# Performance work log

Hardware: AMD Instinct MI355X
Metric: run time of the kernel (lower is better)

The kernel has to match this reference:

```python
import jax, jax.numpy as jnp
import numpy as np

N = 50000      # nodes
E = 800000     # edges
D_IN = 128     # raw feature dim
H = 96         # hidden_channels
K = 8          # experts
L = 4          # num_layers
C = 40         # classes


def setup_inputs() -> dict:
    key = jax.random.key(0)
    ks = jax.random.split(key, 10)
    stdv = 1.0 / np.sqrt(H)
    inp = {
        'x': jax.random.normal(ks[0], (N, D_IN), dtype=jnp.float32),
        'edge_index': jax.random.randint(ks[1], (2, E), 0, N, dtype=jnp.int64),
        # fcs[0]: Linear(d, hidden); fcs[1]: Linear(hidden, c)
        'fc0_w': jax.random.normal(ks[2], (D_IN, H), dtype=jnp.float32) * 0.05,
        'fc0_b': jnp.zeros((H,), dtype=jnp.float32),
        'fc1_w': jax.random.normal(ks[3], (H, C), dtype=jnp.float32) * 0.05,
        'fc1_b': jnp.zeros((C,), dtype=jnp.float32),
        # context_enc (method='node'): per-layer Linear(hidden, K)
        'ctx_w': jax.random.normal(ks[4], (L, H, K), dtype=jnp.float32) * 0.05,
        'ctx_b': jnp.zeros((L, K), dtype=jnp.float32),
        # GraphMultiConvolution weights: [L, K, hidden, hidden], uniform(-stdv, stdv)
        'conv_w': jax.random.uniform(ks[5], (L, K, H, H), dtype=jnp.float32,
                                     minval=-stdv, maxval=stdv),
    }
    return inp


def reference(x, edge_index, fc0_w, fc0_b, fc1_w, fc1_b, ctx_w, ctx_b, conv_w):
    # eval-mode forward (training=False): no dropout, softmax routing
    row = edge_index[0]
    col = edge_index[1]
    h = jax.nn.relu(x @ fc0_w + fc0_b)                     # [N, H]
    for i in range(L):
        # routing logits and soft expert weights z: [N, K]
        z = jax.nn.softmax(h @ ctx_w[i] + ctx_b[i], axis=-1)
        # spmm aggregation: hi[r] = sum over edges (r, c) of h[c]
        hi = jax.ops.segment_sum(h[col], row, num_segments=N)  # [N, H]
        # K-expert batched matmul: [N, K, H]
        outs = jnp.einsum('nd,kdo->nko', hi, conv_w[i])
        # gumbel/softmax-weighted combine + residual
        out = jnp.einsum('nk,nko->no', z, outs) + h
        h = jax.nn.relu(out)
    return h @ fc1_w + fc1_b                               # [N, C]
```

## Files before the change

kernel.cpp:

```cpp
#include <hip/hip_runtime.h>

#define N_NODES 50000
#define N_EDGES 800000
#define DIN     128
#define H       96
#define HS      128
#define K_EXP   8
#define L_LAYERS 4
#define C_OUT   40

#define GSZ 6250

typedef _Float16 f16;
typedef f16 f16x2 __attribute__((ext_vector_type(2)));
typedef f16 f16x4 __attribute__((ext_vector_type(4)));
typedef f16 f16x8 __attribute__((ext_vector_type(8)));
typedef float f32x4 __attribute__((ext_vector_type(4)));


__global__ __launch_bounds__(256) void count_p(const int* __restrict__ row,
                                               int* __restrict__ deg,
                                               int* __restrict__ p, int e) {
    int i = blockIdx.x * blockDim.x + threadIdx.x;
    if (i < e) p[i] = atomicAdd(&deg[row[i]], 1);
}

__global__ __launch_bounds__(1024) void scanA(const int* __restrict__ deg,
                                              int* __restrict__ rowptr,
                                              int* __restrict__ partial, int n) {
    __shared__ int wsum[16];
    int tid  = threadIdx.x;
    int lane = tid & 63, wid = tid >> 6;
    int idx = blockIdx.x * 1024 + tid;
    int v = (idx < n) ? deg[idx] : 0;
    int s = v;
    #pragma unroll
    for (int off = 1; off < 64; off <<= 1) {
        int t = __shfl_up(s, off, 64);
        if (lane >= off) s += t;
    }
    if (lane == 63) wsum[wid] = s;
    __syncthreads();
    if (wid == 0 && lane < 16) {
        int w = wsum[lane];
        #pragma unroll
        for (int off = 1; off < 16; off <<= 1) {
            int t = __shfl_up(w, off, 16);
            if (lane >= off) w += t;
        }
        wsum[lane] = w;
    }
    __syncthreads();
    int waveoff = (wid == 0) ? 0 : wsum[wid - 1];
    if (idx < n) rowptr[idx + 1] = waveoff + s;
    if (tid == 1023) partial[blockIdx.x] = waveoff + s;
}

__global__ __launch_bounds__(1024) void scanC(int* __restrict__ rowptr,
                                              const int* __restrict__ partial,
                                              int nb, int n) {
    __shared__ int boff_s;
    int tid = threadIdx.x;
    if (tid < 64) {
        int v = 0;
        for (int j = tid; j < (int)blockIdx.x; j += 64) v += partial[j];
        #pragma unroll
        for (int off = 32; off >= 1; off >>= 1) v += __shfl_xor(v, off, 64);
        if (tid == 0) boff_s = v;
    }
    __syncthreads();
    int boff = boff_s;
    int idx = blockIdx.x * 1024 + tid;
    if (idx == 0) rowptr[0] = 0;
    if (idx < n) rowptr[idx + 1] += boff;
}

__global__ __launch_bounds__(256) void scatter_store_xcd(const int* __restrict__ row,
                                                         const int* __restrict__ col,
                                                         const int* __restrict__ p,
                                                         const int* __restrict__ rowptr,
                                                         int* __restrict__ csr, int e) {
    int g = blockIdx.x & 7;
    int rlo = g * GSZ, rhi = rlo + GSZ;
    int stride = (gridDim.x >> 3) * 256;
    for (int i = (blockIdx.x >> 3) * 256 + threadIdx.x; i < e; i += stride) {
        int r = row[i];
        if (r >= rlo && r < rhi)
            csr[rowptr[r] + p[i]] = col[i];
    }
}


#define CONV_TOT (L_LAYERS * K_EXP * H * H)
#define FC0_TOT  (DIN * H)
#define FC1_TOT  (48 * H)

__global__ void convert_all(const float* __restrict__ conv_w,
                            const float* __restrict__ fc0_w,
                            const float* __restrict__ fc1_w,
                            f16* __restrict__ wfrag, f16* __restrict__ fc0t,
                            f16* __restrict__ fc1t) {
    int i = blockIdx.x * blockDim.x + threadIdx.x;
    if (i < CONV_TOT) {
        int o = i % H;
        int t = i / H;
        int d = t % H;
        int lk = t / H;
        int ct = o >> 4, lc = o & 15;
        int ks = d >> 5, quad = (d >> 3) & 3, j = d & 7;
        wfrag[(size_t)lk * 9216 + ct * 1536 + ks * 512 + (quad * 16 + lc) * 8 + j] =
            (f16)conv_w[i];
    } else if (i < CONV_TOT + FC0_TOT) {
        int j = i - CONV_TOT;
        int o = j % H, d = j / H;
        fc0t[o * DIN + d] = (f16)fc0_w[j];
    } else if (i < CONV_TOT + FC0_TOT + FC1_TOT) {
        int j = i - CONV_TOT - FC0_TOT;
        int o = j / H, d = j % H;
        fc1t[j] = (o < C_OUT) ? (f16)fc1_w[d * C_OUT + o] : (f16)0.f;
    }
}


#define SPMM_BLOCKS ((N_NODES + 15) / 16)
#define CTX_BLOCKS  ((N_NODES + 255) / 256)

__global__ __launch_bounds__(256) void layer_pre(const f16* __restrict__ h16,
                                                 const int* __restrict__ rowptr,
                                                 const int* __restrict__ csr,
                                                 f16* __restrict__ hi16,
                                                 const float* __restrict__ cw,
                                                 const float* __restrict__ cb,
                                                 float* __restrict__ zt, int n) {
    __shared__ float ws[H * K_EXP];
    __shared__ float bs[K_EXP];
    int tid = threadIdx.x;
    if ((int)blockIdx.x < SPMM_BLOCKS) {
        int r  = blockIdx.x * 16 + (tid >> 4);
        int li = tid & 15;
        if (r >= n) return;
        int j = rowptr[r], e = rowptr[r + 1];
        float acc[8] = {};
        const f16* hb = h16 + li * 8;
        while (j < e) {
            int m = e - j; if (m > 16) m = 16;
            int c = 0;
            if (li < m) c = csr[j + li];
            int t = 0;
            for (; t + 4 <= m; t += 4) {
                int c0 = __shfl(c, t, 16),     c1 = __shfl(c, t + 1, 16);
                int c2 = __shfl(c, t + 2, 16), c3 = __shfl(c, t + 3, 16);
                f16x8 v0 = *(const f16x8*)(hb + (size_t)c0 * HS);
                f16x8 v1 = *(const f16x8*)(hb + (size_t)c1 * HS);
                f16x8 v2 = *(const f16x8*)(hb + (size_t)c2 * HS);
                f16x8 v3 = *(const f16x8*)(hb + (size_t)c3 * HS);
                #pragma unroll
                for (int q = 0; q < 8; q++) acc[q] += (float)v0[q];
                #pragma unroll
                for (int q = 0; q < 8; q++) acc[q] += (float)v1[q];
                #pragma unroll
                for (int q = 0; q < 8; q++) acc[q] += (float)v2[q];
                #pragma unroll
                for (int q = 0; q < 8; q++) acc[q] += (float)v3[q];
            }
            for (; t < m; t++) {
                int cc = __shfl(c, t, 16);
                f16x8 v = *(const f16x8*)(hb + (size_t)cc * HS);
                #pragma unroll
                for (int q = 0; q < 8; q++) acc[q] += (float)v[q];
            }
            j += m;
        }
        if (li < 12) {
            f16x8 o;
            #pragma unroll
            for (int q = 0; q < 8; q++) o[q] = (f16)acc[q];
            *(f16x8*)(hi16 + (size_t)r * HS + li * 8) = o;
        }
    } else {
        for (int t = tid; t < H * K_EXP; t += 256) ws[t] = cw[t];
        if (tid < K_EXP) bs[tid] = cb[tid];
        __syncthreads();
        int node = ((int)blockIdx.x - SPMM_BLOCKS) * 256 + tid;
        if (node >= n) return;
        float acc[K_EXP];
        #pragma unroll
        for (int k = 0; k < K_EXP; k++) acc[k] = bs[k];
        const f16* hr = h16 + (size_t)node * HS;
        #pragma unroll 3
        for (int c8 = 0; c8 < 12; c8++) {
            f16x8 v = *(const f16x8*)(hr + c8 * 8);
            #pragma unroll
            for (int j = 0; j < 8; j++) {
                float hv = (float)v[j];
                int d = c8 * 8 + j;
                #pragma unroll
                for (int k = 0; k < K_EXP; k++) acc[k] += hv * ws[d * K_EXP + k];
            }
        }
        float mx = acc[0];
        #pragma unroll
        for (int k = 1; k < K_EXP; k++) mx = fmaxf(mx, acc[k]);
        float s = 0.f;
        #pragma unroll
        for (int k = 0; k < K_EXP; k++) { acc[k] = __expf(acc[k] - mx); s += acc[k]; }
        float inv = 1.f / s;
        #pragma unroll
        for (int k = 0; k < K_EXP; k++)
            zt[(size_t)k * N_NODES + node] = acc[k] * inv;
    }
}


#define FPAD 136

__global__ __launch_bounds__(256) void fc0_kernel(const float* __restrict__ x,
                                                  const f16* __restrict__ fc0t,
                                                  const float* __restrict__ b,
                                                  f16* __restrict__ h16, int n) {
    __shared__ f16 As[64 * FPAD];
    __shared__ f16 Ws[96 * FPAD];
    int tid = threadIdx.x;
    int l = tid & 63, w = tid >> 6;
    int quad = l >> 4, lc = l & 15;
    int row0 = blockIdx.x * 64;

    for (int t = tid; t < 2048; t += 256) {
        int m = t >> 5, c4 = (t & 31) * 4;
        int gr = row0 + m;
        float4 v = {0.f, 0.f, 0.f, 0.f};
        if (gr < n) v = *(const float4*)(x + (size_t)gr * DIN + c4);
        f16x4 h4 = {(f16)v.x, (f16)v.y, (f16)v.z, (f16)v.w};
        *(f16x4*)&As[m * FPAD + c4] = h4;
    }
    for (int t = tid; t < 1536; t += 256) {
        int o = t >> 4, c8 = (t & 15) * 8;
        *(f16x8*)&Ws[o * FPAD + c8] = *(const f16x8*)(fc0t + o * DIN + c8);
    }
    __syncthreads();

    f16x8 afr[4];
    #pragma unroll
    for (int ks = 0; ks < 4; ks++)
        afr[ks] = *(const f16x8*)&As[(16 * w + lc) * FPAD + ks * 32 + quad * 8];

    f32x4 acc[6] = {};
    #pragma unroll
    for (int ct = 0; ct < 6; ct++) {
        #pragma unroll
        for (int ks = 0; ks < 4; ks++) {
            f16x8 bfr = *(const f16x8*)&Ws[(ct * 16 + lc) * FPAD + ks * 32 + quad * 8];
            acc[ct] = __builtin_amdgcn_mfma_f32_16x16x32_f16(afr[ks], bfr, acc[ct], 0, 0, 0);
        }
    }

    int m0 = 16 * w + quad * 4;
    #pragma unroll
    for (int r = 0; r < 4; r++) {
        int gr = row0 + m0 + r;
        if (gr < n) {
            #pragma unroll
            for (int ct = 0; ct < 6; ct++) {
                int o = ct * 16 + lc;
                h16[(size_t)gr * HS + o] = (f16)fmaxf(acc[ct][r] + b[o], 0.f);
            }
        }
    }
}


#define EG_STAGE 2
#define EG_HALFS (EG_STAGE * 9216)

__global__ __launch_bounds__(256) void expert_gemm(const f16* __restrict__ hi16,
                                                   const f16* __restrict__ hin16,
                                                   const f16* __restrict__ wfrag,
                                                   const float* __restrict__ zt,
                                                   f16* __restrict__ hout16, int n) {
    __shared__ f16 Wl[EG_HALFS];
    int tid = threadIdx.x;
    int l = tid & 63, w = tid >> 6;
    int quad = l >> 4, lc = l & 15;
    int wrow0 = blockIdx.x * 64 + w * 16;

    f16x8 afr[3];
    #pragma unroll
    for (int ks = 0; ks < 3; ks++)
        afr[ks] = *(const f16x8*)(hi16 + (size_t)(wrow0 + lc) * HS + ks * 32 + quad * 8);

    f32x4 acc[6] = {};

    for (int kb = 0; kb < K_EXP; kb += EG_STAGE) {
        __syncthreads();
        const f16* src = wfrag + (size_t)kb * 9216;
        for (int t = tid; t < EG_HALFS / 8; t += 256)
            *(f16x8*)&Wl[t * 8] = *(const f16x8*)(src + t * 8);
        __syncthreads();

        #pragma unroll
        for (int k2 = 0; k2 < EG_STAGE; k2++) {
            int k = kb + k2;
            f32x4 zf = *(const f32x4*)(zt + (size_t)k * N_NODES + wrow0 + quad * 4);
            #pragma unroll
            for (int ct = 0; ct < 6; ct++) {
                f16x8 b0 = *(const f16x8*)&Wl[k2 * 9216 + ct * 1536 + 0 * 512 + l * 8];
                f16x8 b1 = *(const f16x8*)&Wl[k2 * 9216 + ct * 1536 + 1 * 512 + l * 8];
                f16x8 b2 = *(const f16x8*)&Wl[k2 * 9216 + ct * 1536 + 2 * 512 + l * 8];
                f32x4 tmp = {};
                tmp = __builtin_amdgcn_mfma_f32_16x16x32_f16(afr[0], b0, tmp, 0, 0, 0);
                tmp = __builtin_amdgcn_mfma_f32_16x16x32_f16(afr[1], b1, tmp, 0, 0, 0);
                tmp = __builtin_amdgcn_mfma_f32_16x16x32_f16(afr[2], b2, tmp, 0, 0, 0);
                acc[ct] += zf * tmp;
            }
        }
    }

    #pragma unroll
    for (int r = 0; r < 4; r++) {
        int gr = wrow0 + quad * 4 + r;
        if (gr < n) {
            #pragma unroll
            for (int ct = 0; ct < 6; ct++) {
                int o = ct * 16 + lc;
                float v = fmaxf(acc[ct][r] + (float)hin16[(size_t)gr * HS + o], 0.f);
                hout16[(size_t)gr * HS + o] = (f16)v;
            }
        }
    }
}


#define APAD 104

__global__ __launch_bounds__(256) void fc1_kernel(const f16* __restrict__ h16,
                                                  const f16* __restrict__ fc1t,
                                                  const float* __restrict__ b,
                                                  float* __restrict__ out, int n) {
    __shared__ f16 As[64 * APAD];
    __shared__ f16 Ws[48 * APAD];
    int tid = threadIdx.x;
    int l = tid & 63, w = tid >> 6;
    int quad = l >> 4, lc = l & 15;
    int row0 = blockIdx.x * 64;

    for (int t = tid; t < 768; t += 256) {
        int m = t / 12, c8 = (t % 12) * 8;
        int gr = row0 + m;
        f16x8 v = {};
        if (gr < n) v = *(const f16x8*)(h16 + (size_t)gr * HS + c8);
        *(f16x8*)&As[m * APAD + c8] = v;
    }
    for (int t = tid; t < 576; t += 256) {
        int o = t / 12, c8 = (t % 12) * 8;
        *(f16x8*)&Ws[o * APAD + c8] = *(const f16x8*)(fc1t + o * H + c8);
    }
    __syncthreads();

    f16x8 afr[3];
    #pragma unroll
    for (int ks = 0; ks < 3; ks++)
        afr[ks] = *(const f16x8*)&As[(16 * w + lc) * APAD + ks * 32 + quad * 8];

    f32x4 acc[3] = {};
    #pragma unroll
    for (int ct = 0; ct < 3; ct++) {
        #pragma unroll
        for (int ks = 0; ks < 3; ks++) {
            f16x8 bfr = *(const f16x8*)&Ws[(ct * 16 + lc) * APAD + ks * 32 + quad * 8];
            acc[ct] = __builtin_amdgcn_mfma_f32_16x16x32_f16(afr[ks], bfr, acc[ct], 0, 0, 0);
        }
    }

    int m0 = 16 * w + quad * 4;
    #pragma unroll
    for (int r = 0; r < 4; r++) {
        int gr = row0 + m0 + r;
        if (gr < n) {
            #pragma unroll
            for (int ct = 0; ct < 3; ct++) {
                int o = ct * 16 + lc;
                if (o < C_OUT)
                    out[(size_t)gr * C_OUT + o] = acc[ct][r] + b[o];
            }
        }
    }
}


extern "C" void kernel_launch(void* const* d_in, const int* in_sizes, int n_in,
                              void* d_out, int out_size, void* d_ws, size_t ws_size,
                              hipStream_t stream) {
    const float* x      = (const float*)d_in[0];
    const int*   ei     = (const int*)d_in[1];
    const float* fc0_w  = (const float*)d_in[2];
    const float* fc0_b  = (const float*)d_in[3];
    const float* fc1_w  = (const float*)d_in[4];
    const float* fc1_b  = (const float*)d_in[5];
    const float* ctx_w  = (const float*)d_in[6];
    const float* ctx_b  = (const float*)d_in[7];
    const float* conv_w = (const float*)d_in[8];
    float* out = (float*)d_out;

    const size_t NH = (size_t)N_NODES * HS;

    float* zbuf = (float*)d_ws;
    f16*   h16a = (f16*)(zbuf + (size_t)N_NODES * K_EXP);
    f16*   h16b = h16a + NH;
    f16*   hi16 = h16b + NH;
    f16*   wfrag= hi16 + NH;
    f16*   fc0t = wfrag + CONV_TOT;
    f16*   fc1t = fc0t + FC0_TOT;
    int* rowptr = (int*)(fc1t + FC1_TOT);
    int* deg    = rowptr + (N_NODES + 1);
    int* csr    = deg + N_NODES;
    int* prank  = csr + N_EDGES;
    int* partial  = prank + N_EDGES;

    const int* row = ei;
    const int* col = ei + N_EDGES;

    hipMemsetAsync(deg, 0, sizeof(int) * N_NODES, stream);

    count_p<<<(N_EDGES + 255) / 256, 256, 0, stream>>>(row, deg, prank, N_EDGES);
    int nsb = (N_NODES + 1023) / 1024;
    scanA<<<nsb, 1024, 0, stream>>>(deg, rowptr, partial, N_NODES);
    scanC<<<nsb, 1024, 0, stream>>>(rowptr, partial, nsb, N_NODES);
    scatter_store_xcd<<<1024, 256, 0, stream>>>(row, col, prank, rowptr, csr, N_EDGES);

    int ctotal = CONV_TOT + FC0_TOT + FC1_TOT;
    convert_all<<<(ctotal + 255) / 256, 256, 0, stream>>>(conv_w, fc0_w, fc1_w, wfrag, fc0t, fc1t);

    int gemm_grid = (N_NODES + 63) / 64;
    fc0_kernel<<<gemm_grid, 256, 0, stream>>>(x, fc0t, fc0_b, h16a, N_NODES);

    f16* hcur = h16a;
    f16* hnext = h16b;
    for (int i = 0; i < L_LAYERS; i++) {
        layer_pre<<<SPMM_BLOCKS + CTX_BLOCKS, 256, 0, stream>>>(
            hcur, rowptr, csr, hi16,
            ctx_w + (size_t)i * H * K_EXP, ctx_b + (size_t)i * K_EXP, zbuf, N_NODES);
        expert_gemm<<<gemm_grid, 256, 0, stream>>>(
            hi16, hcur, wfrag + (size_t)i * K_EXP * H * H, zbuf, hnext, N_NODES);
        f16* t = hcur; hcur = hnext; hnext = t;
    }
    fc1_kernel<<<gemm_grid, 256, 0, stream>>>(hcur, fc1t, fc1_b, out, N_NODES);
}
```

Baseline: 392.2 us.

## Pack rows densely, use wave-per-row SpMM, 128-row expert tiles, fuse setup kernels

Several independent changes. The node feature row stride drops from 128 to 96 halves, which cuts padded bytes in every gather and GEMM access. SpMM now gives each row a full 64-lane wave that gathers four neighbours at once via readlane and then reduces across lane groups with xor shuffles. The expert GEMM processes 128 rows per block, so each LDS weight fragment is reused for two MFMA row tiles. Degree counting and weight conversion are merged into one launch. Risks: the 96-element stride may leave 16-byte loads misaligned or less coalesced, the doubled accumulators raise register pressure, and low-degree rows leave many SpMM lanes idle.

```diff
diff --git a/kernel.cpp b/kernel.cpp
--- a/kernel.cpp
+++ b/kernel.cpp
@@ -4,7 +4,6 @@
 #define N_EDGES 800000
 #define DIN     128
 #define H       96
-#define HS      128
 #define K_EXP   8
 #define L_LAYERS 4
 #define C_OUT   40
@@ -18,11 +17,46 @@
 typedef float f32x4 __attribute__((ext_vector_type(4)));
 
 
-__global__ __launch_bounds__(256) void count_p(const int* __restrict__ row,
-                                               int* __restrict__ deg,
-                                               int* __restrict__ p, int e) {
-    int i = blockIdx.x * blockDim.x + threadIdx.x;
-    if (i < e) p[i] = atomicAdd(&deg[row[i]], 1);
+#define CONV_TOT (L_LAYERS * K_EXP * H * H)
+#define FC0_TOT  (DIN * H)
+#define FC1_TOT  (48 * H)
+#define CNT_BLOCKS ((N_EDGES + 255) / 256)
+#define CVT_BLOCKS ((CONV_TOT + FC0_TOT + FC1_TOT + 255) / 256)
+
+__global__ __launch_bounds__(256) void count_convert(const int* __restrict__ row,
+                                                     int* __restrict__ deg,
+                                                     int* __restrict__ p,
+                                                     const float* __restrict__ conv_w,
+                                                     const float* __restrict__ fc0_w,
+                                                     const float* __restrict__ fc1_w,
+                                                     f16* __restrict__ wfrag,
+                                                     f16* __restrict__ fc0t,
+                                                     f16* __restrict__ fc1t) {
+    int tid = threadIdx.x;
+    if ((int)blockIdx.x < CNT_BLOCKS) {
+        int i = blockIdx.x * 256 + tid;
+        if (i < N_EDGES) p[i] = atomicAdd(&deg[row[i]], 1);
+    } else {
+        int i = ((int)blockIdx.x - CNT_BLOCKS) * 256 + tid;
+        if (i < CONV_TOT) {
+            int o = i % H;
+            int t = i / H;
+            int d = t % H;
+            int lk = t / H;
+            int ct = o >> 4, lc = o & 15;
+            int ks = d >> 5, quad = (d >> 3) & 3, j = d & 7;
+            wfrag[(size_t)lk * 9216 + ct * 1536 + ks * 512 + (quad * 16 + lc) * 8 + j] =
+                (f16)conv_w[i];
+        } else if (i < CONV_TOT + FC0_TOT) {
+            int j = i - CONV_TOT;
+            int o = j % H, d = j / H;
+            fc0t[o * DIN + d] = (f16)fc0_w[j];
+        } else if (i < CONV_TOT + FC0_TOT + FC1_TOT) {
+            int j = i - CONV_TOT - FC0_TOT;
+            int o = j / H, d = j % H;
+            fc1t[j] = (o < C_OUT) ? (f16)fc1_w[d * C_OUT + o] : (f16)0.f;
+        }
+    }
 }
 
 __global__ __launch_bounds__(1024) void scanA(const int* __restrict__ deg,
@@ -91,38 +125,8 @@
 }
 
 
-#define CONV_TOT (L_LAYERS * K_EXP * H * H)
-#define FC0_TOT  (DIN * H)
-#define FC1_TOT  (48 * H)
-
-__global__ void convert_all(const float* __restrict__ conv_w,
-                            const float* __restrict__ fc0_w,
-                            const float* __restrict__ fc1_w,
-                            f16* __restrict__ wfrag, f16* __restrict__ fc0t,
-                            f16* __restrict__ fc1t) {
-    int i = blockIdx.x * blockDim.x + threadIdx.x;
-    if (i < CONV_TOT) {
-        int o = i % H;
-        int t = i / H;
-        int d = t % H;
-        int lk = t / H;
-        int ct = o >> 4, lc = o & 15;
-        int ks = d >> 5, quad = (d >> 3) & 3, j = d & 7;
-        wfrag[(size_t)lk * 9216 + ct * 1536 + ks * 512 + (quad * 16 + lc) * 8 + j] =
-            (f16)conv_w[i];
-    } else if (i < CONV_TOT + FC0_TOT) {
-        int j = i - CONV_TOT;
-        int o = j % H, d = j / H;
-        fc0t[o * DIN + d] = (f16)fc0_w[j];
-    } else if (i < CONV_TOT + FC0_TOT + FC1_TOT) {
-        int j = i - CONV_TOT - FC0_TOT;
-        int o = j / H, d = j % H;
-        fc1t[j] = (o < C_OUT) ? (f16)fc1_w[d * C_OUT + o] : (f16)0.f;
-    }
-}
-
-
-#define SPMM_BLOCKS ((N_NODES + 15) / 16)
+#define SPMM_WPB 4
+#define SPMM_BLOCKS ((N_NODES + SPMM_WPB - 1) / SPMM_WPB)
 #define CTX_BLOCKS  ((N_NODES + 255) / 256)
 
 __global__ __launch_bounds__(256) void layer_pre(const f16* __restrict__ h16,
@@ -136,46 +140,57 @@
     __shared__ float bs[K_EXP];
     int tid = threadIdx.x;
     if ((int)blockIdx.x < SPMM_BLOCKS) {
-        int r  = blockIdx.x * 16 + (tid >> 4);
-        int li = tid & 15;
+        int wid  = tid >> 6;
+        int lane = tid & 63;
+        int r = blockIdx.x * SPMM_WPB + wid;
         if (r >= n) return;
+        int q16 = lane >> 4;
+        int li  = lane & 15;
+        bool act_l = li < 12;
         int j = rowptr[r], e = rowptr[r + 1];
         float acc[8] = {};
-        const f16* hb = h16 + li * 8;
-        while (j < e) {
-            int m = e - j; if (m > 16) m = 16;
+        const size_t lane_off = (size_t)li * 8;
+        for (int jb = j; jb < e; jb += 64) {
+            int m = e - jb; if (m > 64) m = 64;
             int c = 0;
-            if (li < m) c = csr[j + li];
-            int t = 0;
-            for (; t + 4 <= m; t += 4) {
-                int c0 = __shfl(c, t, 16),     c1 = __shfl(c, t + 1, 16);
-                int c2 = __shfl(c, t + 2, 16), c3 = __shfl(c, t + 3, 16);
-                f16x8 v0 = *(const f16x8*)(hb + (size_t)c0 * HS);
-                f16x8 v1 = *(const f16x8*)(hb + (size_t)c1 * HS);
-                f16x8 v2 = *(const f16x8*)(hb + (size_t)c2 * HS);
-                f16x8 v3 = *(const f16x8*)(hb + (size_t)c3 * HS);
-                #pragma unroll
-                for (int q = 0; q < 8; q++) acc[q] += (float)v0[q];
-                #pragma unroll
-                for (int q = 0; q < 8; q++) acc[q] += (float)v1[q];
-                #pragma unroll
-                for (int q = 0; q < 8; q++) acc[q] += (float)v2[q];
-                #pragma unroll
-                for (int q = 0; q < 8; q++) acc[q] += (float)v3[q];
-            }
-            for (; t < m; t++) {
-                int cc = __shfl(c, t, 16);
-                f16x8 v = *(const f16x8*)(hb + (size_t)cc * HS);
-                #pragma unroll
-                for (int q = 0; q < 8; q++) acc[q] += (float)v[q];
-            }
-            j += m;
-        }
-        if (li < 12) {
+            if (lane < m) c = csr[jb + lane];
+            for (int t = 0; t < m; t += 8) {
+                int a0 = __builtin_amdgcn_readlane(c, t);
+                int a1 = __builtin_amdgcn_readlane(c, t + 1);
+                int a2 = __builtin_amdgcn_readlane(c, t + 2);
+                int a3 = __builtin_amdgcn_readlane(c, t + 3);
+                int ca = q16 == 0 ? a0 : q16 == 1 ? a1 : q16 == 2 ? a2 : a3;
+                bool actA = act_l && (t + q16 < m);
+                f16x8 vA = {};
+                if (actA) vA = *(const f16x8*)(h16 + (size_t)ca * H + lane_off);
+                int b0 = __builtin_amdgcn_readlane(c, t + 4);
+                int b1 = __builtin_amdgcn_readlane(c, t + 5);
+                int b2 = __builtin_amdgcn_readlane(c, t + 6);
+                int b3 = __builtin_amdgcn_readlane(c, t + 7);
+                int cbx = q16 == 0 ? b0 : q16 == 1 ? b1 : q16 == 2 ? b2 : b3;
+                bool actB = act_l && (t + 4 + q16 < m);
+                f16x8 vB = {};
+                if (actB) vB = *(const f16x8*)(h16 + (size_t)cbx * H + lane_off);
+                if (actA) {
+                    #pragma unroll
+                    for (int q = 0; q < 8; q++) acc[q] += (float)vA[q];
+                }
+                if (actB) {
+                    #pragma unroll
+                    for (int q = 0; q < 8; q++) acc[q] += (float)vB[q];
+                }
+            }
+        }
+        #pragma unroll
+        for (int q = 0; q < 8; q++) {
+            acc[q] += __shfl_xor(acc[q], 32, 64);
+            acc[q] += __shfl_xor(acc[q], 16, 64);
+        }
+        if (lane < 12) {
             f16x8 o;
             #pragma unroll
             for (int q = 0; q < 8; q++) o[q] = (f16)acc[q];
-            *(f16x8*)(hi16 + (size_t)r * HS + li * 8) = o;
+            *(f16x8*)(hi16 + (size_t)r * H + lane * 8) = o;
         }
     } else {
         for (int t = tid; t < H * K_EXP; t += 256) ws[t] = cw[t];
@@ -186,7 +201,7 @@
         float acc[K_EXP];
         #pragma unroll
         for (int k = 0; k < K_EXP; k++) acc[k] = bs[k];
-        const f16* hr = h16 + (size_t)node * HS;
+        const f16* hr = h16 + (size_t)node * H;
         #pragma unroll 3
         for (int c8 = 0; c8 < 12; c8++) {
             f16x8 v = *(const f16x8*)(hr + c8 * 8);
@@ -262,7 +277,7 @@
             #pragma unroll
             for (int ct = 0; ct < 6; ct++) {
                 int o = ct * 16 + lc;
-                h16[(size_t)gr * HS + o] = (f16)fmaxf(acc[ct][r] + b[o], 0.f);
+                h16[(size_t)gr * H + o] = (f16)fmaxf(acc[ct][r] + b[o], 0.f);
             }
         }
     }
@@ -281,14 +296,19 @@
     int tid = threadIdx.x;
     int l = tid & 63, w = tid >> 6;
     int quad = l >> 4, lc = l & 15;
-    int wrow0 = blockIdx.x * 64 + w * 16;
-
-    f16x8 afr[3];
-    #pragma unroll
-    for (int ks = 0; ks < 3; ks++)
-        afr[ks] = *(const f16x8*)(hi16 + (size_t)(wrow0 + lc) * HS + ks * 32 + quad * 8);
-
-    f32x4 acc[6] = {};
+    int brow = blockIdx.x * 128;
+    int wrow0 = brow + w * 16;
+    int wrow1 = wrow0 + 64;
+
+    f16x8 afr0[3], afr1[3];
+    #pragma unroll
+    for (int ks = 0; ks < 3; ks++) {
+        afr0[ks] = *(const f16x8*)(hi16 + (size_t)(wrow0 + lc) * H + ks * 32 + quad * 8);
+        afr1[ks] = *(const f16x8*)(hi16 + (size_t)(wrow1 + lc) * H + ks * 32 + quad * 8);
+    }
+
+    f32x4 acc0[6] = {};
+    f32x4 acc1[6] = {};
 
     for (int kb = 0; kb < K_EXP; kb += EG_STAGE) {
         __syncthreads();
@@ -300,30 +320,45 @@
         #pragma unroll
         for (int k2 = 0; k2 < EG_STAGE; k2++) {
             int k = kb + k2;
-            f32x4 zf = *(const f32x4*)(zt + (size_t)k * N_NODES + wrow0 + quad * 4);
+            f32x4 zf0 = *(const f32x4*)(zt + (size_t)k * N_NODES + wrow0 + quad * 4);
+            f32x4 zf1 = *(const f32x4*)(zt + (size_t)k * N_NODES + wrow1 + quad * 4);
             #pragma unroll
             for (int ct = 0; ct < 6; ct++) {
                 f16x8 b0 = *(const f16x8*)&Wl[k2 * 9216 + ct * 1536 + 0 * 512 + l * 8];
                 f16x8 b1 = *(const f16x8*)&Wl[k2 * 9216 + ct * 1536 + 1 * 512 + l * 8];
                 f16x8 b2 = *(const f16x8*)&Wl[k2 * 9216 + ct * 1536 + 2 * 512 + l * 8];
-                f32x4 tmp = {};
-                tmp = __builtin_amdgcn_mfma_f32_16x16x32_f16(afr[0], b0, tmp, 0, 0, 0);
-                tmp = __builtin_amdgcn_mfma_f32_16x16x32_f16(afr[1], b1, tmp, 0, 0, 0);
-                tmp = __builtin_amdgcn_mfma_f32_16x16x32_f16(afr[2], b2, tmp, 0, 0, 0);
-                acc[ct] += zf * tmp;
+                f32x4 t0 = {};
+                t0 = __builtin_amdgcn_mfma_f32_16x16x32_f16(afr0[0], b0, t0, 0, 0, 0);
+                t0 = __builtin_amdgcn_mfma_f32_16x16x32_f16(afr0[1], b1, t0, 0, 0, 0);
+                t0 = __builtin_amdgcn_mfma_f32_16x16x32_f16(afr0[2], b2, t0, 0, 0, 0);
+                acc0[ct] += zf0 * t0;
+                f32x4 t1 = {};
+                t1 = __builtin_amdgcn_mfma_f32_16x16x32_f16(afr1[0], b0, t1, 0, 0, 0);
+                t1 = __builtin_amdgcn_mfma_f32_16x16x32_f16(afr1[1], b1, t1, 0, 0, 0);
+                t1 = __builtin_amdgcn_mfma_f32_16x16x32_f16(afr1[2], b2, t1, 0, 0, 0);
+                acc1[ct] += zf1 * t1;
             }
         }
     }
 
     #pragma unroll
     for (int r = 0; r < 4; r++) {
-        int gr = wrow0 + quad * 4 + r;
-        if (gr < n) {
+        int gr0 = wrow0 + quad * 4 + r;
+        if (gr0 < n) {
             #pragma unroll
             for (int ct = 0; ct < 6; ct++) {
                 int o = ct * 16 + lc;
-                float v = fmaxf(acc[ct][r] + (float)hin16[(size_t)gr * HS + o], 0.f);
-                hout16[(size_t)gr * HS + o] = (f16)v;
+                float v = fmaxf(acc0[ct][r] + (float)hin16[(size_t)gr0 * H + o], 0.f);
+                hout16[(size_t)gr0 * H + o] = (f16)v;
+            }
+        }
+        int gr1 = wrow1 + quad * 4 + r;
+        if (gr1 < n) {
+            #pragma unroll
+            for (int ct = 0; ct < 6; ct++) {
+                int o = ct * 16 + lc;
+                float v = fmaxf(acc1[ct][r] + (float)hin16[(size_t)gr1 * H + o], 0.f);
+                hout16[(size_t)gr1 * H + o] = (f16)v;
             }
         }
     }
@@ -347,7 +382,7 @@
         int m = t / 12, c8 = (t % 12) * 8;
         int gr = row0 + m;
         f16x8 v = {};
-        if (gr < n) v = *(const f16x8*)(h16 + (size_t)gr * HS + c8);
+        if (gr < n) v = *(const f16x8*)(h16 + (size_t)gr * H + c8);
         *(f16x8*)&As[m * APAD + c8] = v;
     }
     for (int t = tid; t < 576; t += 256) {
@@ -401,7 +436,7 @@
     const float* conv_w = (const float*)d_in[8];
     float* out = (float*)d_out;
 
-    const size_t NH = (size_t)N_NODES * HS;
+    const size_t NH = (size_t)N_NODES * H;
 
     float* zbuf = (float*)d_ws;
     f16*   h16a = (f16*)(zbuf + (size_t)N_NODES * K_EXP);
@@ -421,25 +456,24 @@
 
     hipMemsetAsync(deg, 0, sizeof(int) * N_NODES, stream);
 
-    count_p<<<(N_EDGES + 255) / 256, 256, 0, stream>>>(row, deg, prank, N_EDGES);
+    count_convert<<<CNT_BLOCKS + CVT_BLOCKS, 256, 0, stream>>>(
+        row, deg, prank, conv_w, fc0_w, fc1_w, wfrag, fc0t, fc1t);
     int nsb = (N_NODES + 1023) / 1024;
     scanA<<<nsb, 1024, 0, stream>>>(deg, rowptr, partial, N_NODES);
     scanC<<<nsb, 1024, 0, stream>>>(rowptr, partial, nsb, N_NODES);
     scatter_store_xcd<<<1024, 256, 0, stream>>>(row, col, prank, rowptr, csr, N_EDGES);
 
-    int ctotal = CONV_TOT + FC0_TOT + FC1_TOT;
-    convert_all<<<(ctotal + 255) / 256, 256, 0, stream>>>(conv_w, fc0_w, fc1_w, wfrag, fc0t, fc1t);
-
     int gemm_grid = (N_NODES + 63) / 64;
     fc0_kernel<<<gemm_grid, 256, 0, stream>>>(x, fc0t, fc0_b, h16a, N_NODES);
 
+    int eg_grid = (N_NODES + 127) / 128;
     f16* hcur = h16a;
     f16* hnext = h16b;
     for (int i = 0; i < L_LAYERS; i++) {
         layer_pre<<<SPMM_BLOCKS + CTX_BLOCKS, 256, 0, stream>>>(
             hcur, rowptr, csr, hi16,
             ctx_w + (size_t)i * H * K_EXP, ctx_b + (size_t)i * K_EXP, zbuf, N_NODES);
-        expert_gemm<<<gemm_grid, 256, 0, stream>>>(
+        expert_gemm<<<eg_grid, 256, 0, stream>>>(
             hi16, hcur, wfrag + (size_t)i * K_EXP * H * H, zbuf, hnext, N_NODES);
         f16* t = hcur; hcur = hnext; hnext = t;
     }
```

Result: slower. 426.3 us (+8.7%).
